# Kernel tuning notes

Measured on AMD Instinct MI355X. Metric: run time of the kernel, lower is better.

Reference implementation:

```python
import jax, jax.numpy as jnp
import numpy as np

K = 1024          # num_embeddings
D = 768           # embedding_dim
COMMIT = 0.25     # commitment_cost
PW = 0.1          # perplexity_weight


def setup_inputs() -> dict:
    key = jax.random.key(0)
    k1, k2 = jax.random.split(key)
    inputs = jax.random.normal(k1, (32, 2048, D), dtype=jnp.float32)
    weight = jax.random.normal(k2, (K, D), dtype=jnp.float32)  # codebook
    return {"inputs": inputs, "weight": weight}


def reference(inputs, weight):
    """Eval-mode forward of VectorQuantizerEMA (deterministic nearest-code lookup)."""
    in_shape = inputs.shape
    flat = inputs.reshape(-1, D)                       # [N, D]
    valid = jnp.linalg.norm(flat, axis=1) > 1e-6       # padding mask [N]
    maskf = valid.astype(flat.dtype)
    n_valid = maskf.sum()

    dist = (jnp.sum(flat * flat, axis=1, keepdims=True)
            + jnp.sum(weight * weight, axis=1)
            - 2.0 * flat @ weight.T)

    idx = jnp.argmin(dist, axis=1)                     # [N]
    min_d = jnp.min(dist, axis=1)                      # [N]
    idx = jnp.where(valid, idx, 0)
    min_d = jnp.where(valid, min_d, 0.0)

    q_flat = weight[idx] * maskf[:, None]              # zeros at padded rows
    quantized = q_flat.reshape(in_shape)
    quantized_st = inputs + jax.lax.stop_gradient(quantized - inputs)

    # commitment loss: MSE over valid rows only
    sq_err = jnp.sum((flat - jax.lax.stop_gradient(q_flat)) ** 2, axis=1)
    loss_commit = jnp.sum(maskf * sq_err) / (n_valid * D)

    # perplexity over valid assignments (one-hot mean == normalized counts)
    counts = jnp.zeros((K,), flat.dtype).at[idx].add(maskf)
    avg_probs = counts / n_valid
    perplexity = jnp.exp(-jnp.sum(avg_probs * jnp.log(avg_probs + 1e-10)))
    perplexity_loss = -jnp.log(perplexity + 1e-10)

    total_loss = COMMIT * loss_commit + PW * perplexity_loss

    indices = idx.reshape(in_shape[:-1])
    min_distances = min_d.reshape(in_shape[:-1])
    return quantized_st, total_loss, indices, min_distances, perplexity
```

## Files before the change

### kernel.cpp

```cpp
#include <hip/hip_runtime.h>
#include <hip/hip_bf16.h>
#include <math.h>

#define NROWS 65536
#define DDIM  768
#define KCODES 1024
#define NCB   8
#define BM    128
#define BK    128
#define KC    32
#define NCH   (DDIM / KC)
#define BK2   32
#define NCH2  (DDIM / BK2)
#define PANEL_USH (24 * 4096)
#define GAP_TAU  0.3f
#define FILT_TAU 0.6f
#define RGRID 2048
#define QGRID 2048

#define OUT_LOSS ((size_t)NROWS * DDIM)
#define OUT_IDX  (OUT_LOSS + 1)
#define OUT_MIND (OUT_IDX + NROWS)
#define OUT_PERP (OUT_MIND + NROWS)

#define WS_SUM    0
#define WS_NSUS   8
#define WS_NVAL   12
#define WS_COUNTS 256
#define WS_WSQ    (WS_COUNTS + 4*KCODES)
#define WS_ROWS   (WS_WSQ + 4*KCODES)
#define WS_ROWI   (WS_ROWS + 4*NROWS)
#define WS_SUSP   (WS_ROWI + 4*NROWS)
#define WS_PM1    (WS_SUSP + 4*NROWS)
#define WS_PM2    (WS_PM1 + (size_t)4*NROWS*NCB)
#define WS_PIDX   (WS_PM2 + (size_t)4*NROWS*NCB)
#define WS_END    (WS_PIDX + (size_t)4*NROWS*NCB)
#define WS_AF16   ((WS_END + 255) & ~(size_t)255)
#define WS_WF16   (WS_AF16 + (size_t)NROWS * DDIM * 2)
#define WS_END2   (WS_WF16 + (size_t)KCODES * DDIM * 2)

typedef __attribute__((ext_vector_type(8))) _Float16 half8;
typedef __attribute__((ext_vector_type(4))) float f32x4;

#define GLOAD16(gsrc, ldst) \
    __builtin_amdgcn_global_load_lds( \
        (const __attribute__((address_space(1))) unsigned int*)(gsrc), \
        (__attribute__((address_space(3))) unsigned int*)(ldst), 16, 0, 0)

template <typename T>
__device__ inline T waveRedAdd(T v) {
#pragma unroll
    for (int o = 32; o; o >>= 1) v += __shfl_xor(v, o);
    return v;
}

__device__ inline ushort f2h(float f) {
    union { _Float16 h; ushort u; } c;
    c.h = (_Float16)f;
    return c.u;
}

__global__ void k_init(float* counts, int* n_suspect, unsigned* n_valid, double* sum_sqerr) {
    const int t = threadIdx.x;
    if (t == 0) { *n_suspect = 0; *n_valid = 0u; *sum_sqerr = 0.0; }
    for (int k = t; k < KCODES; k += 256) counts[k] = 0.f;
}

#define ASLOTS (NROWS * (DDIM / 8))
#define TSLOTS ((NROWS + KCODES) * (DDIM / 8))
__global__ __launch_bounds__(256) void k_convert(
    const float* __restrict__ A, const float* __restrict__ W,
    ushort* __restrict__ Af16, ushort* __restrict__ Wf16)
{
    for (int gidx = blockIdx.x * 256 + threadIdx.x; gidx < TSLOTS; gidx += gridDim.x * 256) {
        const float* src; ushort* dst; int sid;
        if (gidx < ASLOTS) { src = A; dst = Af16; sid = gidx; }
        else { src = W; dst = Wf16; sid = gidx - ASLOTS; }
        const int row = sid / 96;
        const int sl = sid - row * 96;
        const int ch = sl >> 2, s = sl & 3;
        const float* p = src + (size_t)row * DDIM + ch * 32 + s * 8;
        const float4 a = *(const float4*)p;
        const float4 b = *(const float4*)(p + 4);
        uint4 v;
        v.x = ((unsigned)f2h(a.y) << 16) | f2h(a.x);
        v.y = ((unsigned)f2h(a.w) << 16) | f2h(a.z);
        v.z = ((unsigned)f2h(b.y) << 16) | f2h(b.x);
        v.w = ((unsigned)f2h(b.w) << 16) | f2h(b.z);
        const size_t dsti = (size_t)(row >> 7) * PANEL_USH + ch * 4096
                          + (row & 127) * 32 + ((s ^ ((row >> 1) & 3)) << 3);
        *(uint4*)(dst + dsti) = v;
    }
}

__global__ __launch_bounds__(256) void k_wsq(const float* __restrict__ W, float* __restrict__ wsq) {
    const int k = blockIdx.x;
    const int t = threadIdx.x;
    const float* w = W + (size_t)k * DDIM;
    const float a = w[t], b = w[t + 256], c = w[t + 512];
    float s = a * a + b * b + c * c;
    s = waveRedAdd(s);
    __shared__ float p[4];
    if ((t & 63) == 0) p[t >> 6] = s;
    __syncthreads();
    if (t == 0) wsq[k] = (p[0] + p[1]) + (p[2] + p[3]);
}

__global__ __launch_bounds__(256, 4) void k_partials_g(
    const ushort* __restrict__ Af16, const ushort* __restrict__ Wf16,
    const float* __restrict__ wsq,
    float* __restrict__ pm1, float* __restrict__ pm2, int* __restrict__ pidx)
{
    __shared__ __align__(16) ushort lds[2 * 2 * BM * BK2];

    const int bid = blockIdx.x;
    const int rb = ((bid & 7) << 6) | (bid >> 6);
    const int cb = (bid >> 3) & 7;

    const int tid = threadIdx.x;
    const int wid = tid >> 6, lane = tid & 63;
    const int wr = wid >> 1, wc = wid & 1;
    const int l15 = lane & 15, g = lane >> 4;

    const ushort* Ap = Af16 + (size_t)rb * PANEL_USH;
    const ushort* Wp = Wf16 + (size_t)cb * PANEL_USH;

    int aoff[4], boff[4];
#pragma unroll
    for (int rt = 0; rt < 4; ++rt) {
        const int r = wr * 64 + rt * 16 + l15;
        aoff[rt] = r * 32 + ((g ^ ((r >> 1) & 3)) << 3);
        const int c = wc * 64 + rt * 16 + l15;
        boff[rt] = c * 32 + ((g ^ ((c >> 1) & 3)) << 3);
    }

    f32x4 acc[4][4];
#pragma unroll
    for (int rt = 0; rt < 4; ++rt)
#pragma unroll
        for (int ct = 0; ct < 4; ++ct) acc[rt][ct] = (f32x4)0.f;

    const int lseg = lane << 3;
    auto STAGE = [&](int ch, int b) {
        ushort* As = lds + b * 8192;
        ushort* Ws = As + 4096;
        const ushort* Asrc = Ap + ch * 4096;
        const ushort* Wsrc = Wp + ch * 4096;
        GLOAD16(Asrc + (wid << 9) + lseg,       (char*)As + (wid << 10));
        GLOAD16(Asrc + ((wid + 4) << 9) + lseg, (char*)As + ((wid + 4) << 10));
        GLOAD16(Wsrc + (wid << 9) + lseg,       (char*)Ws + (wid << 10));
        GLOAD16(Wsrc + ((wid + 4) << 9) + lseg, (char*)Ws + ((wid + 4) << 10));
    };

    STAGE(0, 0);
    STAGE(1, 1);
    asm volatile("s_waitcnt vmcnt(4)" ::: "memory");
    __builtin_amdgcn_s_barrier();

#pragma unroll 1
    for (int ch = 0; ch < NCH2; ++ch) {
        const int cur = ch & 1;
        const ushort* As = lds + cur * 8192;
        const ushort* Ws = As + 4096;
        half8 bf[4];
#pragma unroll
        for (int ct = 0; ct < 4; ++ct) bf[ct] = *(const half8*)(Ws + boff[ct]);
#pragma unroll
        for (int rt = 0; rt < 4; ++rt) {
            const half8 af = *(const half8*)(As + aoff[rt]);
#pragma unroll
            for (int ct = 0; ct < 4; ++ct)
                acc[rt][ct] = __builtin_amdgcn_mfma_f32_16x16x32_f16(af, bf[ct], acc[rt][ct], 0, 0, 0);
        }
        if (ch + 1 == NCH2) break;
        asm volatile("s_waitcnt lgkmcnt(0)" ::: "memory");
        __builtin_amdgcn_s_barrier();
        if (ch + 2 < NCH2) {
            STAGE(ch + 2, cur);
            asm volatile("s_waitcnt vmcnt(4)" ::: "memory");
        } else {
            asm volatile("s_waitcnt vmcnt(0)" ::: "memory");
        }
        __builtin_amdgcn_s_barrier();
    }
    __syncthreads();

    float wq[4];
#pragma unroll
    for (int ct = 0; ct < 4; ++ct) wq[ct] = wsq[cb * BK + wc * 64 + ct * 16 + l15];
    const int cbase = cb * BK + wc * 64 + l15;

    float* tm1 = (float*)lds;
    float* tm2 = tm1 + 256;
    int*   ti1 = (int*)(tm2 + 256);

#pragma unroll
    for (int rt = 0; rt < 4; ++rt) {
        float m1q[4], m2q[4]; int i1q[4];
#pragma unroll
        for (int q = 0; q < 4; ++q) { m1q[q] = INFINITY; m2q[q] = INFINITY; i1q[q] = 0x7fffffff; }
#pragma unroll
        for (int ct = 0; ct < 4; ++ct) {
            const int col = cbase + ct * 16;
#pragma unroll
            for (int q = 0; q < 4; ++q) {
                const float s = fmaf(-2.f, acc[rt][ct][q], wq[ct]);
                if (s < m1q[q]) { m2q[q] = m1q[q]; m1q[q] = s; i1q[q] = col; }
                else if (s < m2q[q]) m2q[q] = s;
            }
        }
#pragma unroll
        for (int msk = 1; msk <= 8; msk <<= 1) {
#pragma unroll
            for (int q = 0; q < 4; ++q) {
                const float om1 = __shfl_xor(m1q[q], msk);
                const float om2 = __shfl_xor(m2q[q], msk);
                const int   oi1 = __shfl_xor(i1q[q], msk);
                if (om1 < m1q[q] || (om1 == m1q[q] && oi1 < i1q[q])) {
                    m2q[q] = fminf(m1q[q], om2); m1q[q] = om1; i1q[q] = oi1;
                } else m2q[q] = fminf(m2q[q], om1);
            }
        }
        if (l15 == 0) {
#pragma unroll
            for (int q = 0; q < 4; ++q) {
                const int rl = wr * 64 + rt * 16 + g * 4 + q;
                tm1[rl * 2 + wc] = m1q[q];
                tm2[rl * 2 + wc] = m2q[q];
                ti1[rl * 2 + wc] = i1q[q];
            }
        }
    }
    __syncthreads();
    if (tid < BM) {
        float m1 = tm1[tid * 2], m2 = tm2[tid * 2]; int i1 = ti1[tid * 2];
        const float bm1 = tm1[tid * 2 + 1], bm2 = tm2[tid * 2 + 1]; const int bi = ti1[tid * 2 + 1];
        if (bm1 < m1 || (bm1 == m1 && bi < i1)) { m2 = fminf(m1, bm2); m1 = bm1; i1 = bi; }
        else m2 = fminf(m2, bm1);
        const size_t row = (size_t)rb * BM + tid;
        pm1[row * NCB + cb] = m1;
        pm2[row * NCB + cb] = m2;
        pidx[row * NCB + cb] = i1;
    }
}

__global__ __launch_bounds__(256, 2) void k_partials(
    const float* __restrict__ A, const float* __restrict__ W,
    const float* __restrict__ wsq,
    float* __restrict__ pm1, float* __restrict__ pm2, int* __restrict__ pidx)
{
    __shared__ __align__(16) ushort lds[2 * BM * KC];
    ushort* As = lds;
    ushort* Ws = lds + BM * KC;

    const int bid = blockIdx.x;
    const int rb = ((bid & 7) << 6) | (bid >> 6);
    const int cb = (bid >> 3) & 7;

    const int tid = threadIdx.x;
    const int wid = tid >> 6, lane = tid & 63;
    const int wr = wid >> 1, wc = wid & 1;
    const int l15 = lane & 15, g = lane >> 4;

    const float* Ab = A + (size_t)rb * BM * DDIM;
    const float* Wb = W + (size_t)cb * BK * DDIM;

    const int srow = tid >> 3;
    const int sk4  = (tid & 7) << 2;
    const int sg   = (tid & 7) >> 1;
    const int sh   = (tid & 1) << 2;

    int aOff[4], bOff[4];
#pragma unroll
    for (int rt = 0; rt < 4; ++rt) {
        const int r = wr * 64 + rt * 16 + l15;
        aOff[rt] = r * KC + ((g ^ ((r >> 1) & 3)) << 3);
        const int c = wc * 64 + rt * 16 + l15;
        bOff[rt] = c * KC + ((g ^ ((c >> 1) & 3)) << 3);
    }

    f32x4 acc[4][4];
#pragma unroll
    for (int rt = 0; rt < 4; ++rt)
#pragma unroll
        for (int ct = 0; ct < 4; ++ct) acc[rt][ct] = (f32x4)0.f;

    float4 av[4], wv[4];
#pragma unroll
    for (int i = 0; i < 4; ++i) {
        av[i] = *(const float4*)(Ab + (size_t)(srow + 32 * i) * DDIM + sk4);
        wv[i] = *(const float4*)(Wb + (size_t)(srow + 32 * i) * DDIM + sk4);
    }

#pragma unroll 1
    for (int ch = 0; ch < NCH; ++ch) {
        __syncthreads();
#pragma unroll
        for (int i = 0; i < 4; ++i) {
            const int r = srow + 32 * i;
            const int wsl = r * KC + ((sg ^ ((r >> 1) & 3)) << 3) + sh;
            ushort4 ua; ua.x = f2h(av[i].x); ua.y = f2h(av[i].y); ua.z = f2h(av[i].z); ua.w = f2h(av[i].w);
            *(ushort4*)(As + wsl) = ua;
            ushort4 uw; uw.x = f2h(wv[i].x); uw.y = f2h(wv[i].y); uw.z = f2h(wv[i].z); uw.w = f2h(wv[i].w);
            *(ushort4*)(Ws + wsl) = uw;
        }
        __syncthreads();
        if (ch + 1 < NCH) {
            const int d0 = (ch + 1) * KC + sk4;
#pragma unroll
            for (int i = 0; i < 4; ++i) {
                av[i] = *(const float4*)(Ab + (size_t)(srow + 32 * i) * DDIM + d0);
                wv[i] = *(const float4*)(Wb + (size_t)(srow + 32 * i) * DDIM + d0);
            }
        }
        half8 af[4], bf[4];
#pragma unroll
        for (int rt = 0; rt < 4; ++rt) af[rt] = *(const half8*)(As + aOff[rt]);
#pragma unroll
        for (int ct = 0; ct < 4; ++ct) bf[ct] = *(const half8*)(Ws + bOff[ct]);
#pragma unroll
        for (int rt = 0; rt < 4; ++rt)
#pragma unroll
            for (int ct = 0; ct < 4; ++ct)
                acc[rt][ct] = __builtin_amdgcn_mfma_f32_16x16x32_f16(af[rt], bf[ct], acc[rt][ct], 0, 0, 0);
    }

    float wq[4];
#pragma unroll
    for (int ct = 0; ct < 4; ++ct) wq[ct] = wsq[cb * BK + wc * 64 + ct * 16 + l15];
    const int cbase = cb * BK + wc * 64 + l15;

    __syncthreads();
    float* tm1 = (float*)lds;
    float* tm2 = tm1 + 256;
    int*   ti1 = (int*)(tm2 + 256);

#pragma unroll
    for (int rt = 0; rt < 4; ++rt) {
        float m1q[4], m2q[4]; int i1q[4];
#pragma unroll
        for (int q = 0; q < 4; ++q) { m1q[q] = INFINITY; m2q[q] = INFINITY; i1q[q] = 0x7fffffff; }
#pragma unroll
        for (int ct = 0; ct < 4; ++ct) {
            const int col = cbase + ct * 16;
#pragma unroll
            for (int q = 0; q < 4; ++q) {
                const float s = fmaf(-2.f, acc[rt][ct][q], wq[ct]);
                if (s < m1q[q]) { m2q[q] = m1q[q]; m1q[q] = s; i1q[q] = col; }
                else if (s < m2q[q]) m2q[q] = s;
            }
        }
#pragma unroll
        for (int msk = 1; msk <= 8; msk <<= 1) {
#pragma unroll
            for (int q = 0; q < 4; ++q) {
                const float om1 = __shfl_xor(m1q[q], msk);
                const float om2 = __shfl_xor(m2q[q], msk);
                const int   oi1 = __shfl_xor(i1q[q], msk);
                if (om1 < m1q[q] || (om1 == m1q[q] && oi1 < i1q[q])) {
                    m2q[q] = fminf(m1q[q], om2); m1q[q] = om1; i1q[q] = oi1;
                } else m2q[q] = fminf(m2q[q], om1);
            }
        }
        if (l15 == 0) {
#pragma unroll
            for (int q = 0; q < 4; ++q) {
                const int rl = wr * 64 + rt * 16 + g * 4 + q;
                tm1[rl * 2 + wc] = m1q[q];
                tm2[rl * 2 + wc] = m2q[q];
                ti1[rl * 2 + wc] = i1q[q];
            }
        }
    }
    __syncthreads();
    if (tid < BM) {
        float m1 = tm1[tid * 2], m2 = tm2[tid * 2]; int i1 = ti1[tid * 2];
        const float bm1 = tm1[tid * 2 + 1], bm2 = tm2[tid * 2 + 1]; const int bi = ti1[tid * 2 + 1];
        if (bm1 < m1 || (bm1 == m1 && bi < i1)) { m2 = fminf(m1, bm2); m1 = bm1; i1 = bi; }
        else m2 = fminf(m2, bm1);
        const size_t row = (size_t)rb * BM + tid;
        pm1[row * NCB + cb] = m1;
        pm2[row * NCB + cb] = m2;
        pidx[row * NCB + cb] = i1;
    }
}

__global__ __launch_bounds__(256) void k_merge(
    const float* __restrict__ pm1, const float* __restrict__ pm2, const int* __restrict__ pidx,
    float* __restrict__ row_s, int* __restrict__ row_idx,
    int* __restrict__ suspects, int* __restrict__ n_suspect)
{
    const int row = blockIdx.x * 256 + threadIdx.x;
    float m1 = INFINITY, m2 = INFINITY; int i1 = 0x7fffffff;
#pragma unroll
    for (int cb = 0; cb < NCB; ++cb) {
        const float bm1 = pm1[(size_t)row * NCB + cb];
        const float bm2 = pm2[(size_t)row * NCB + cb];
        const int   bi  = pidx[(size_t)row * NCB + cb];
        if (bm1 < m1 || (bm1 == m1 && bi < i1)) { m2 = fminf(m1, bm2); m1 = bm1; i1 = bi; }
        else m2 = fminf(m2, bm1);
    }
    row_s[row] = m1;
    row_idx[row] = i1;
    if (m2 - m1 < GAP_TAU) {
        const int p = atomicAdd(n_suspect, 1);
        suspects[p] = row;
    }
}

__global__ __launch_bounds__(256) void k_repair(
    const float* __restrict__ A, const float* __restrict__ W,
    const float* __restrict__ pm1,
    const int* __restrict__ suspects, const int* __restrict__ n_suspect,
    float* __restrict__ row_s, int* __restrict__ row_idx)
{
    __shared__ __align__(16) float xrow[DDIM];
    __shared__ double wbest[4]; __shared__ int wbi[4];
    __shared__ double xps[4];
    __shared__ int qcb[NCB];
    __shared__ int nq;
    const int ns = *n_suspect;
    const int tid = threadIdx.x;
    const int wid = tid >> 6, lane = tid & 63;
    const int sub = tid & 3;
    const int cq  = tid >> 2;

    for (int s = blockIdx.x; s < ns; s += gridDim.x) {
        const int row = suspects[s];
        __syncthreads();
        xrow[tid]       = A[(size_t)row * DDIM + tid];
        xrow[tid + 256] = A[(size_t)row * DDIM + tid + 256];
        xrow[tid + 512] = A[(size_t)row * DDIM + tid + 512];
        if (tid == 0) {
            float gmin = INFINITY;
#pragma unroll
            for (int cb = 0; cb < NCB; ++cb) gmin = fminf(gmin, pm1[(size_t)row * NCB + cb]);
            int n = 0;
#pragma unroll
            for (int cb = 0; cb < NCB; ++cb)
                if (pm1[(size_t)row * NCB + cb] <= gmin + FILT_TAU) qcb[n++] = cb;
            nq = n;
        }
        __syncthreads();

        double xp = 0.0;
        {
            double t;
            t = (double)xrow[tid];       xp = fma(t, t, xp);
            t = (double)xrow[tid + 256]; xp = fma(t, t, xp);
            t = (double)xrow[tid + 512]; xp = fma(t, t, xp);
        }
        xp = waveRedAdd(xp);
        if (lane == 0) xps[wid] = xp;

        double best = 1e300; int bi = 0x7fffffff;
        const int ncand = nq * BK;
        for (int base = 0; base < ncand; base += 64) {
            const int ci = base + cq;
            const bool act = ci < ncand;
            double d = 0.0; int k = 0x7fffffff;
            if (act) {
                k = qcb[ci >> 7] * BK + (ci & (BK - 1));
                const float* wr = W + (size_t)k * DDIM + (sub << 2);
                const float* xr = xrow + (sub << 2);
                double d0 = 0.0, d1 = 0.0;
                for (int i = 0; i < DDIM; i += 16) {
                    const float4 wv = *(const float4*)(wr + i);
                    const float4 xv = *(const float4*)(xr + i);
                    double t;
                    t = (double)xv.x - (double)wv.x; d0 = fma(t, t, d0);
                    t = (double)xv.y - (double)wv.y; d1 = fma(t, t, d1);
                    t = (double)xv.z - (double)wv.z; d0 = fma(t, t, d0);
                    t = (double)xv.w - (double)wv.w; d1 = fma(t, t, d1);
                }
                d = d0 + d1;
            }
            d += __shfl_xor(d, 1);
            d += __shfl_xor(d, 2);
            if (act && sub == 0) {
                if (d < best || (d == best && k < bi)) { best = d; bi = k; }
            }
        }
#pragma unroll
        for (int o = 32; o; o >>= 1) {
            const double ob = __shfl_xor(best, o);
            const int oi = __shfl_xor(bi, o);
            if (ob < best || (ob == best && oi < bi)) { best = ob; bi = oi; }
        }
        if (lane == 0) { wbest[wid] = best; wbi[wid] = bi; }
        __syncthreads();
        if (tid == 0) {
            double b = wbest[0]; int i1 = wbi[0];
#pragma unroll
            for (int w = 1; w < 4; ++w)
                if (wbest[w] < b || (wbest[w] == b && wbi[w] < i1)) { b = wbest[w]; i1 = wbi[w]; }
            row_idx[row] = i1;
            row_s[row] = (float)(b - (xps[0] + xps[1] + xps[2] + xps[3]));
        }
    }
}

__global__ __launch_bounds__(256) void k_quantize(
    const float* __restrict__ A, const float* __restrict__ W,
    const float* __restrict__ row_s, const int* __restrict__ row_idx,
    float* __restrict__ out, float* __restrict__ counts,
    unsigned int* __restrict__ n_valid, double* __restrict__ sum_sqerr)
{
    const int wid = threadIdx.x >> 6, lane = threadIdx.x & 63;
    __shared__ double s_sum[4];
    __shared__ unsigned s_val[4];
    double wsum = 0.0; unsigned wval = 0;

#pragma unroll 1
    for (int it = 0; it < NROWS / (QGRID * 4); ++it) {
        const int row = (it * QGRID + blockIdx.x) * 4 + wid;
        const float* x = A + (size_t)row * DDIM;
        float4 xv[3];
#pragma unroll
        for (int j = 0; j < 3; ++j) xv[j] = *(const float4*)(x + (lane + 64 * j) * 4);
        float xsq = 0.f;
#pragma unroll
        for (int j = 0; j < 3; ++j)
            xsq += xv[j].x * xv[j].x + xv[j].y * xv[j].y + xv[j].z * xv[j].z + xv[j].w * xv[j].w;
        xsq = waveRedAdd(xsq);
        const bool valid = xsq > 1e-12f;
        const float maskf = valid ? 1.f : 0.f;
        const int idx = row_idx[row];
        const int idxm = valid ? idx : 0;
        const float* w = W + (size_t)idx * DDIM;
        float* oq = out + (size_t)row * DDIM;
        float e2 = 0.f;
#pragma unroll
        for (int j = 0; j < 3; ++j) {
            const float4 wvv = *(const float4*)(w + (lane + 64 * j) * 4);
            const float xs[4] = {xv[j].x, xv[j].y, xv[j].z, xv[j].w};
            const float ws[4] = {wvv.x, wvv.y, wvv.z, wvv.w};
            float os[4];
#pragma unroll
            for (int c = 0; c < 4; ++c) {
                const float q = ws[c] * maskf;
                os[c] = xs[c] + (q - xs[c]);
                const float d = xs[c] - q;
                e2 += d * d;
            }
            float4 ov; ov.x = os[0]; ov.y = os[1]; ov.z = os[2]; ov.w = os[3];
            *(float4*)(oq + (lane + 64 * j) * 4) = ov;
        }
        e2 = waveRedAdd(e2);
        if (lane == 0) {
            wsum += (double)(maskf * e2);
            if (valid) {
                ++wval;
                atomicAdd(&counts[idxm], 1.0f);
            }
            out[OUT_IDX + row]  = (float)idxm;
            out[OUT_MIND + row] = valid ? (xsq + row_s[row]) : 0.f;
        }
    }

    if (lane == 0) { s_sum[wid] = wsum; s_val[wid] = wval; }
    __syncthreads();
    if (threadIdx.x == 0) {
        atomicAdd(sum_sqerr, s_sum[0] + s_sum[1] + s_sum[2] + s_sum[3]);
        atomicAdd(n_valid, s_val[0] + s_val[1] + s_val[2] + s_val[3]);
    }
}

__global__ __launch_bounds__(256) void k_final(
    const float* __restrict__ counts, const unsigned int* __restrict__ n_valid,
    const double* __restrict__ sum_sqerr, float* __restrict__ out)
{
    const int t = threadIdx.x;
    const float nv = (float)(*n_valid);
    double ent = 0.0;
    for (int k = t; k < KCODES; k += 256) {
        const float p = counts[k] / nv;
        ent += (double)(p * logf(p + 1e-10f));
    }
    ent = waveRedAdd(ent);
    __shared__ double ps[4];
    if ((t & 63) == 0) ps[t >> 6] = ent;
    __syncthreads();
    if (t == 0) {
        const double e = ps[0] + ps[1] + ps[2] + ps[3];
        const double perp = exp(-e);
        const double ploss = -log(perp + 1e-10);
        const double commit = *sum_sqerr / ((double)(*n_valid) * (double)DDIM);
        out[OUT_LOSS] = (float)(0.25 * commit + 0.1 * ploss);
        out[OUT_PERP] = (float)perp;
    }
}

extern "C" void kernel_launch(void* const* d_in, const int* in_sizes, int n_in,
                              void* d_out, int out_size, void* d_ws, size_t ws_size,
                              hipStream_t stream) {
    const float* A = (const float*)d_in[0];
    const float* W = (const float*)d_in[1];
    float* out = (float*)d_out;
    char* ws = (char*)d_ws;
    if (ws_size < (size_t)WS_END) return;

    double*   sum_sqerr = (double*)(ws + WS_SUM);
    int*      n_suspect = (int*)(ws + WS_NSUS);
    unsigned* n_valid   = (unsigned*)(ws + WS_NVAL);
    float*    counts    = (float*)(ws + WS_COUNTS);
    float*    wsq       = (float*)(ws + WS_WSQ);
    float*    row_s     = (float*)(ws + WS_ROWS);
    int*      row_idx   = (int*)(ws + WS_ROWI);
    int*      suspects  = (int*)(ws + WS_SUSP);
    float*    pm1       = (float*)(ws + WS_PM1);
    float*    pm2       = (float*)(ws + WS_PM2);
    int*      pidx      = (int*)(ws + WS_PIDX);
    ushort*   Af16      = (ushort*)(ws + WS_AF16);
    ushort*   Wf16      = (ushort*)(ws + WS_WF16);

    const bool big = ws_size >= (size_t)WS_END2;

    hipLaunchKernelGGL(k_init, dim3(1), dim3(256), 0, stream, counts, n_suspect, n_valid, sum_sqerr);
    if (big)
        hipLaunchKernelGGL(k_convert, dim3(2048), dim3(256), 0, stream, A, W, Af16, Wf16);
    hipLaunchKernelGGL(k_wsq, dim3(KCODES), dim3(256), 0, stream, W, wsq);
    if (big)
        hipLaunchKernelGGL(k_partials_g, dim3((NROWS / BM) * NCB), dim3(256), 0, stream, Af16, Wf16, wsq, pm1, pm2, pidx);
    else
        hipLaunchKernelGGL(k_partials, dim3((NROWS / BM) * NCB), dim3(256), 0, stream, A, W, wsq, pm1, pm2, pidx);
    hipLaunchKernelGGL(k_merge, dim3(NROWS / 256), dim3(256), 0, stream, pm1, pm2, pidx, row_s, row_idx, suspects, n_suspect);
    hipLaunchKernelGGL(k_repair, dim3(RGRID), dim3(256), 0, stream, A, W, pm1, suspects, n_suspect, row_s, row_idx);
    hipLaunchKernelGGL(k_quantize, dim3(QGRID), dim3(256), 0, stream, A, W, row_s, row_idx, out, counts, n_valid, sum_sqerr);
    hipLaunchKernelGGL(k_final, dim3(1), dim3(256), 0, stream, counts, n_valid, sum_sqerr, out);
}
```

Before: 368.1 us.

## Compute row norms during fp16 conversion and drop input re-read in quantize

The fp16 conversion kernel now also computes each input row's squared norm (192-thread blocks so that each pass covers exactly two rows) and stores it in a new workspace array. The quantize kernel no longer reads the 200MB input again: it writes the selected codebook row directly as the straight-through output and takes the commitment error from the min-distance value (xsq + row_s) instead of recomputing it. MFMA sections also get raised wave priority via s_setprio. The risks are small numeric differences in the output (x+(q-x) versus q) and in the loss from using the expanded-distance formula, plus two barriers per loop iteration in the conversion kernel.

```diff
diff --git a/kernel.cpp b/kernel.cpp
--- a/kernel.cpp
+++ b/kernel.cpp
@@ -28,7 +28,8 @@
 #define WS_NVAL   12
 #define WS_COUNTS 256
 #define WS_WSQ    (WS_COUNTS + 4*KCODES)
-#define WS_ROWS   (WS_WSQ + 4*KCODES)
+#define WS_XSQ    (WS_WSQ + 4*KCODES)
+#define WS_ROWS   (WS_XSQ + 4*NROWS)
 #define WS_ROWI   (WS_ROWS + 4*NROWS)
 #define WS_SUSP   (WS_ROWI + 4*NROWS)
 #define WS_PM1    (WS_SUSP + 4*NROWS)
@@ -66,16 +67,51 @@
     for (int k = t; k < KCODES; k += 256) counts[k] = 0.f;
 }
 
+__global__ __launch_bounds__(256) void k_wsq(const float* __restrict__ W, float* __restrict__ wsq) {
+    const int k = blockIdx.x;
+    const int t = threadIdx.x;
+    const float* w = W + (size_t)k * DDIM;
+    const float a = w[t], b = w[t + 256], c = w[t + 512];
+    float s = a * a + b * b + c * c;
+    s = waveRedAdd(s);
+    __shared__ float p[4];
+    if ((t & 63) == 0) p[t >> 6] = s;
+    __syncthreads();
+    if (t == 0) wsq[k] = (p[0] + p[1]) + (p[2] + p[3]);
+}
+
+__global__ __launch_bounds__(256) void k_xsq(const float* __restrict__ A, float* __restrict__ xsq) {
+    const int wid = threadIdx.x >> 6, lane = threadIdx.x & 63;
+    const int row = blockIdx.x * 4 + wid;
+    const float* x = A + (size_t)row * DDIM;
+    float s = 0.f;
+#pragma unroll
+    for (int j = 0; j < 3; ++j) {
+        const float4 v = *(const float4*)(x + (lane + 64 * j) * 4);
+        s += v.x * v.x + v.y * v.y + v.z * v.z + v.w * v.w;
+    }
+    s = waveRedAdd(s);
+    if (lane == 0) xsq[row] = s;
+}
+
 #define ASLOTS (NROWS * (DDIM / 8))
 #define TSLOTS ((NROWS + KCODES) * (DDIM / 8))
-__global__ __launch_bounds__(256) void k_convert(
+__global__ __launch_bounds__(192) void k_convert(
     const float* __restrict__ A, const float* __restrict__ W,
-    ushort* __restrict__ Af16, ushort* __restrict__ Wf16)
+    ushort* __restrict__ Af16, ushort* __restrict__ Wf16,
+    float* __restrict__ xsq)
 {
-    for (int gidx = blockIdx.x * 256 + threadIdx.x; gidx < TSLOTS; gidx += gridDim.x * 256) {
-        const float* src; ushort* dst; int sid;
-        if (gidx < ASLOTS) { src = A; dst = Af16; sid = gidx; }
-        else { src = W; dst = Wf16; sid = gidx - ASLOTS; }
+    __shared__ float part[4];
+    const int t = threadIdx.x;
+    const int wv = t >> 6;
+
+#pragma unroll 1
+    for (size_t base = (size_t)blockIdx.x * 192; base < (size_t)TSLOTS; base += (size_t)gridDim.x * 192) {
+        const size_t gidx = base + t;
+        const bool isA = base < (size_t)ASLOTS;
+        const float* src = isA ? A : W;
+        ushort* dst = isA ? Af16 : Wf16;
+        const int sid = (int)(gidx - (isA ? 0 : (size_t)ASLOTS));
         const int row = sid / 96;
         const int sl = sid - row * 96;
         const int ch = sl >> 2, s = sl & 3;
@@ -90,20 +126,29 @@
         const size_t dsti = (size_t)(row >> 7) * PANEL_USH + ch * 4096
                           + (row & 127) * 32 + ((s ^ ((row >> 1) & 3)) << 3);
         *(uint4*)(dst + dsti) = v;
-    }
-}
-
-__global__ __launch_bounds__(256) void k_wsq(const float* __restrict__ W, float* __restrict__ wsq) {
-    const int k = blockIdx.x;
-    const int t = threadIdx.x;
-    const float* w = W + (size_t)k * DDIM;
-    const float a = w[t], b = w[t + 256], c = w[t + 512];
-    float s = a * a + b * b + c * c;
-    s = waveRedAdd(s);
-    __shared__ float p[4];
-    if ((t & 63) == 0) p[t >> 6] = s;
-    __syncthreads();
-    if (t == 0) wsq[k] = (p[0] + p[1]) + (p[2] + p[3]);
+
+        if (isA) {
+            float sq = a.x * a.x + a.y * a.y + a.z * a.z + a.w * a.w
+                     + b.x * b.x + b.y * b.y + b.z * b.z + b.w * b.w;
+            if (wv == 1) {
+#pragma unroll
+                for (int o = 16; o; o >>= 1) sq += __shfl_xor(sq, o);
+            } else {
+                sq = waveRedAdd(sq);
+            }
+            if (t == 0)   part[0] = sq;
+            if (t == 64)  part[1] = sq;
+            if (t == 96)  part[2] = sq;
+            if (t == 128) part[3] = sq;
+            __syncthreads();
+            if (t == 0) {
+                const int r0 = (int)(base / 96);
+                xsq[r0]     = part[0] + part[1];
+                xsq[r0 + 1] = part[2] + part[3];
+            }
+            __syncthreads();
+        }
+    }
 }
 
 __global__ __launch_bounds__(256, 4) void k_partials_g(
@@ -165,6 +210,7 @@
         half8 bf[4];
 #pragma unroll
         for (int ct = 0; ct < 4; ++ct) bf[ct] = *(const half8*)(Ws + boff[ct]);
+        __builtin_amdgcn_s_setprio(1);
 #pragma unroll
         for (int rt = 0; rt < 4; ++rt) {
             const half8 af = *(const half8*)(As + aoff[rt]);
@@ -172,6 +218,7 @@
             for (int ct = 0; ct < 4; ++ct)
                 acc[rt][ct] = __builtin_amdgcn_mfma_f32_16x16x32_f16(af, bf[ct], acc[rt][ct], 0, 0, 0);
         }
+        __builtin_amdgcn_s_setprio(0);
         if (ch + 1 == NCH2) break;
         asm volatile("s_waitcnt lgkmcnt(0)" ::: "memory");
         __builtin_amdgcn_s_barrier();
@@ -501,7 +548,8 @@
 }
 
 __global__ __launch_bounds__(256) void k_quantize(
-    const float* __restrict__ A, const float* __restrict__ W,
+    const float* __restrict__ W,
+    const float* __restrict__ xsq,
     const float* __restrict__ row_s, const int* __restrict__ row_idx,
     float* __restrict__ out, float* __restrict__ counts,
     unsigned int* __restrict__ n_valid, double* __restrict__ sum_sqerr)
@@ -514,47 +562,27 @@
 #pragma unroll 1
     for (int it = 0; it < NROWS / (QGRID * 4); ++it) {
         const int row = (it * QGRID + blockIdx.x) * 4 + wid;
-        const float* x = A + (size_t)row * DDIM;
-        float4 xv[3];
-#pragma unroll
-        for (int j = 0; j < 3; ++j) xv[j] = *(const float4*)(x + (lane + 64 * j) * 4);
-        float xsq = 0.f;
-#pragma unroll
-        for (int j = 0; j < 3; ++j)
-            xsq += xv[j].x * xv[j].x + xv[j].y * xv[j].y + xv[j].z * xv[j].z + xv[j].w * xv[j].w;
-        xsq = waveRedAdd(xsq);
-        const bool valid = xsq > 1e-12f;
-        const float maskf = valid ? 1.f : 0.f;
+        const float xs = xsq[row];
+        const bool valid = xs > 1e-12f;
         const int idx = row_idx[row];
         const int idxm = valid ? idx : 0;
         const float* w = W + (size_t)idx * DDIM;
         float* oq = out + (size_t)row * DDIM;
-        float e2 = 0.f;
 #pragma unroll
         for (int j = 0; j < 3; ++j) {
-            const float4 wvv = *(const float4*)(w + (lane + 64 * j) * 4);
-            const float xs[4] = {xv[j].x, xv[j].y, xv[j].z, xv[j].w};
-            const float ws[4] = {wvv.x, wvv.y, wvv.z, wvv.w};
-            float os[4];
-#pragma unroll
-            for (int c = 0; c < 4; ++c) {
-                const float q = ws[c] * maskf;
-                os[c] = xs[c] + (q - xs[c]);
-                const float d = xs[c] - q;
-                e2 += d * d;
-            }
-            float4 ov; ov.x = os[0]; ov.y = os[1]; ov.z = os[2]; ov.w = os[3];
-            *(float4*)(oq + (lane + 64 * j) * 4) = ov;
-        }
-        e2 = waveRedAdd(e2);
+            float4 wv = *(const float4*)(w + (lane + 64 * j) * 4);
+            if (!valid) { wv.x = 0.f; wv.y = 0.f; wv.z = 0.f; wv.w = 0.f; }
+            *(float4*)(oq + (lane + 64 * j) * 4) = wv;
+        }
         if (lane == 0) {
-            wsum += (double)(maskf * e2);
+            const float mind = xs + row_s[row];
             if (valid) {
+                wsum += (double)mind;
                 ++wval;
                 atomicAdd(&counts[idxm], 1.0f);
             }
             out[OUT_IDX + row]  = (float)idxm;
-            out[OUT_MIND + row] = valid ? (xsq + row_s[row]) : 0.f;
+            out[OUT_MIND + row] = valid ? mind : 0.f;
         }
     }
 
@@ -605,6 +633,7 @@
     unsigned* n_valid   = (unsigned*)(ws + WS_NVAL);
     float*    counts    = (float*)(ws + WS_COUNTS);
     float*    wsq       = (float*)(ws + WS_WSQ);
+    float*    xsq       = (float*)(ws + WS_XSQ);
     float*    row_s     = (float*)(ws + WS_ROWS);
     int*      row_idx   = (int*)(ws + WS_ROWI);
     int*      suspects  = (int*)(ws + WS_SUSP);
@@ -617,15 +646,16 @@
     const bool big = ws_size >= (size_t)WS_END2;
 
     hipLaunchKernelGGL(k_init, dim3(1), dim3(256), 0, stream, counts, n_suspect, n_valid, sum_sqerr);
-    if (big)
-        hipLaunchKernelGGL(k_convert, dim3(2048), dim3(256), 0, stream, A, W, Af16, Wf16);
     hipLaunchKernelGGL(k_wsq, dim3(KCODES), dim3(256), 0, stream, W, wsq);
-    if (big)
+    if (big) {
+        hipLaunchKernelGGL(k_convert, dim3(2048), dim3(192), 0, stream, A, W, Af16, Wf16, xsq);
         hipLaunchKernelGGL(k_partials_g, dim3((NROWS / BM) * NCB), dim3(256), 0, stream, Af16, Wf16, wsq, pm1, pm2, pidx);
-    else
+    } else {
+        hipLaunchKernelGGL(k_xsq, dim3(NROWS / 4), dim3(256), 0, stream, A, xsq);
         hipLaunchKernelGGL(k_partials, dim3((NROWS / BM) * NCB), dim3(256), 0, stream, A, W, wsq, pm1, pm2, pidx);
+    }
     hipLaunchKernelGGL(k_merge, dim3(NROWS / 256), dim3(256), 0, stream, pm1, pm2, pidx, row_s, row_idx, suspects, n_suspect);
     hipLaunchKernelGGL(k_repair, dim3(RGRID), dim3(256), 0, stream, A, W, pm1, suspects, n_suspect, row_s, row_idx);
-    hipLaunchKernelGGL(k_quantize, dim3(QGRID), dim3(256), 0, stream, A, W, row_s, row_idx, out, counts, n_valid, sum_sqerr);
+    hipLaunchKernelGGL(k_quantize, dim3(QGRID), dim3(256), 0, stream, W, xsq, row_s, row_idx, out, counts, n_valid, sum_sqerr);
     hipLaunchKernelGGL(k_final, dim3(1), dim3(256), 0, stream, counts, n_valid, sum_sqerr, out);
 }
```

Result: no change. 364.5 us (-1.0%).
